# Kernel tuning notes

Measured on AMD Instinct MI355X. Metric: run time of the kernel, lower is better.

The kernel has to match this reference:

```python
import jax, jax.numpy as jnp
import numpy as np

INF_NUMBER = 1.0e12
ZERO_TOL = 1e-9
NEG_SLOPE = 0.2

B, G, N = 16, 128, 512
P, E, K, F = 4, 1, 3, 128


def setup_inputs() -> dict:
    key = jax.random.key(0)
    k1, k2, k3, k4, k5, k6, k7 = jax.random.split(key, 7)
    x = jax.random.normal(k1, (B, G, N), dtype=jnp.float32)
    u = jax.random.uniform(k2, (B, E, N, N), dtype=jnp.float32)
    S = jnp.where(u < 0.1, u, 0.0)
    std = 1.0 / np.sqrt(G * P)
    W = jax.random.uniform(k3, (P, E, G, G), minval=-std, maxval=std, dtype=jnp.float32)
    mixer = jax.random.uniform(k4, (P, E, 2 * F), minval=-std, maxval=std, dtype=jnp.float32)
    h = jax.random.uniform(k5, (P, F, E, K, G), minval=-std, maxval=std, dtype=jnp.float32)
    b = jax.random.uniform(k6, (F, 1), minval=-std, maxval=std, dtype=jnp.float32)
    return {"x": x, "S": S, "W": W, "mixer": mixer, "h": h, "b": b}


def _attention_gso(x, W, S):
    # x: (B,G,N); W: (P,E,G,G); S: (B,E,N,N)
    # Wx = W @ x_query : (B,P,E,G,N)
    Wx = jnp.einsum('pegh,bhn->bpegn', W, x)
    # xWx = x_key @ Wx : (B,P,E,N,N)  (x_key[b,m,g] = x[b,g,m])
    xWx = jnp.einsum('bgm,bpegn->bpemn', x, Wx)
    eij = jax.nn.leaky_relu(xWx, negative_slope=NEG_SLOPE)
    # edge mask from |S| summed over edge features: (B,1,1,N,N)
    mask = (jnp.sum(jnp.abs(S), axis=1) > ZERO_TOL).astype(x.dtype)[:, None, None]
    scores = eij * mask - (1.0 - mask) * INF_NUMBER
    aij = jax.nn.softmax(scores, axis=-1) * mask
    return aij  # (B,P,E,N,N)


def reference(x, S, W, mixer, h, b):
    # mixer is declared by the torch module but unused in key-query mode
    aij = _attention_gso(x, W, S)  # (B,P,E,N,N)
    # K-hop taps: z[k] = x @ aij^k, broadcast over (P,E)
    xk = jnp.broadcast_to(x[:, None, None], (B, P, E, G, N))
    taps = [xk]
    for _ in range(1, K):
        xk = jnp.einsum('bpegn,bpenm->bpegm', xk, aij)
        taps.append(xk)
    z = jnp.stack(taps, axis=3)  # (B,P,E,K,G,N)
    # filter GEMM: contract over (E,K,G) -> (B,P,F,N)
    y = jnp.einsum('bpekgn,pfekg->bpfn', z, h) + b  # b: (F,1) broadcasts
    # concatenate heads: relu then (B, P*F, N)
    y = jax.nn.relu(y)
    y = jnp.transpose(y, (0, 3, 1, 2)).reshape(B, N, P * F)
    return jnp.transpose(y, (0, 2, 1))
```

## Files before the change

kernel.cpp:

```cpp
#include <hip/hip_runtime.h>

#define Bx 16
#define Gx 128
#define Nx 512
#define Px 4
#define Kx 3
#define Fx 128
#define NEG_SLOPE 0.2f
#define ZERO_TOL 1e-9f
#define BIGF 1.0e30f

typedef unsigned short u16;
typedef unsigned int u32;
typedef __bf16 v8bf __attribute__((ext_vector_type(8)));
typedef _Float16 v8hf __attribute__((ext_vector_type(8)));
typedef float v4f __attribute__((ext_vector_type(4)));

__device__ __forceinline__ u16 f2b(float f) {
  union { float f; u32 u; } v; v.f = f;
  u32 r = (v.u + 0x7fffu + ((v.u >> 16) & 1u)) >> 16;
  return (u16)r;
}
__device__ __forceinline__ u16 f2h(float f) {
  union { _Float16 h; u16 u; } v; v.h = (_Float16)f;
  return v.u;
}

#define G2L16(gsrc, ldst)                                                     \
  __builtin_amdgcn_global_load_lds(                                           \
      (const __attribute__((address_space(1))) void*)(gsrc),                  \
      (__attribute__((address_space(3))) void*)(ldst), 16, 0, 0)

__global__ __launch_bounds__(256) void mask_kernel(const float* __restrict__ S,
                                                   u32* __restrict__ mb) {
  const int wi = blockIdx.x * 256 + threadIdx.x;
  const float4* S4 = (const float4*)S;
  u32 bits = 0;
#pragma unroll
  for (int q = 0; q < 8; q++) {
    float4 v = S4[(size_t)wi * 8 + q];
    bits |= (fabsf(v.x) > ZERO_TOL ? 1u : 0u) << (q * 4);
    bits |= (fabsf(v.y) > ZERO_TOL ? 2u : 0u) << (q * 4);
    bits |= (fabsf(v.z) > ZERO_TOL ? 4u : 0u) << (q * 4);
    bits |= (fabsf(v.w) > ZERO_TOL ? 8u : 0u) << (q * 4);
  }
  mb[wi] = bits;
}

__global__ __launch_bounds__(256) void castx3_kernel(const float* __restrict__ x,
                                                     u16* __restrict__ xb,
                                                     u16* __restrict__ xTb,
                                                     u16* __restrict__ xT16) {
  const int b = blockIdx.z, g0 = blockIdx.x * 32, n0 = blockIdx.y * 32;
  const int tid = threadIdx.x;
  __shared__ float t[32][33];
  const int r = tid >> 3, c4 = (tid & 7) * 4;
  const float* xp = x + (size_t)b * Gx * Nx;
  float4 v = *(const float4*)&xp[(g0 + r) * Nx + n0 + c4];
  ushort4 o;
  o.x = f2b(v.x); o.y = f2b(v.y); o.z = f2b(v.z); o.w = f2b(v.w);
  *(ushort4*)&xb[(size_t)b * Gx * Nx + (g0 + r) * Nx + n0 + c4] = o;
  t[r][c4 + 0] = v.x; t[r][c4 + 1] = v.y; t[r][c4 + 2] = v.z; t[r][c4 + 3] = v.w;
  __syncthreads();
  float tv[4] = {t[c4 + 0][r], t[c4 + 1][r], t[c4 + 2][r], t[c4 + 3][r]};
  ushort4 ob, oh;
  ob.x = f2b(tv[0]); oh.x = f2h(tv[0]);
  ob.y = f2b(tv[1]); oh.y = f2h(tv[1]);
  ob.z = f2b(tv[2]); oh.z = f2h(tv[2]);
  ob.w = f2b(tv[3]); oh.w = f2h(tv[3]);
  size_t off = (size_t)b * Nx * Gx + (size_t)(n0 + r) * Gx + g0 + c4;
  *(ushort4*)&xTb[off] = ob;
  *(ushort4*)&xT16[off] = oh;
}

__global__ __launch_bounds__(256) void castw16_kernel(const float* __restrict__ W,
                                                      u16* __restrict__ w16) {
  int i4 = (blockIdx.x * 256 + threadIdx.x) * 4;
  float4 v = *(const float4*)&W[i4];
  ushort4 o;
  o.x = f2h(v.x); o.y = f2h(v.y); o.z = f2h(v.z); o.w = f2h(v.w);
  *(ushort4*)&w16[i4] = o;
}

__global__ __launch_bounds__(256) void casth_kernel(const float* __restrict__ h,
                                                    u16* __restrict__ Hb) {
  int i4 = (blockIdx.x * 256 + threadIdx.x) * 4;
  float4 v = *(const float4*)&h[i4];
  ushort4 o;
  o.x = f2b(v.x); o.y = f2b(v.y); o.z = f2b(v.z); o.w = f2b(v.w);
  *(ushort4*)&Hb[i4] = o;
}

__global__ __launch_bounds__(256) void wxt16_kernel(const u16* __restrict__ xT16,
                                                    const u16* __restrict__ w16,
                                                    u16* __restrict__ WxT16) {
  __shared__ __align__(16) char smem[49152];
  constexpr int OB = 16384;
  const int bp = blockIdx.x, b = bp >> 2, p = bp & 3;
  const int rt = blockIdx.y;
  const int tid = threadIdx.x;
  const int w = tid >> 6, l = tid & 63;
  const int wr = w >> 1, wc = w & 1;
  const int lr = l & 15, ks = l >> 4;

  const u16* Ap = xT16 + ((size_t)b * Nx + rt * 64) * Gx;
  const u16* Bp = w16 + (size_t)p * Gx * Gx;
#pragma unroll
  for (int it = 0; it < 4; it++) {
    int chunk = it * 256 + w * 64 + l;
    int r = chunk >> 4, kq = l & 15;
    int kg = (kq ^ (r & 15)) * 8;
    G2L16(Ap + (size_t)r * Gx + kg, smem + it * 4096 + w * 1024);
  }
#pragma unroll
  for (int it = 0; it < 8; it++) {
    int chunk = it * 256 + w * 64 + l;
    int r = chunk >> 4, kq = l & 15;
    int kg = (kq ^ (r & 15)) * 8;
    G2L16(Bp + (size_t)r * Gx + kg, smem + OB + it * 4096 + w * 1024);
  }
  __syncthreads();

  v4f acc[2][4];
#pragma unroll
  for (int fr = 0; fr < 2; fr++)
#pragma unroll
    for (int fc = 0; fc < 4; fc++) acc[fr][fc] = (v4f){0.f, 0.f, 0.f, 0.f};

#pragma unroll
  for (int t = 0; t < 4; t++) {
    int kk = t * 4 + ks;
    v8hf ah[2];
#pragma unroll
    for (int fr = 0; fr < 2; fr++) {
      int ra = wr * 32 + fr * 16 + lr;
      ah[fr] = *(const v8hf*)(smem + ra * 256 + ((kk ^ (ra & 15)) * 16));
    }
#pragma unroll
    for (int fc = 0; fc < 4; fc++) {
      int rb = wc * 64 + fc * 16 + lr;
      v8hf bh = *(const v8hf*)(smem + OB + rb * 256 + ((kk ^ (rb & 15)) * 16));
#pragma unroll
      for (int fr = 0; fr < 2; fr++)
        acc[fr][fc] = __builtin_amdgcn_mfma_f32_16x16x32_f16(ah[fr], bh, acc[fr][fc], 0, 0, 0);
    }
  }

  u16* op = WxT16 + (size_t)bp * Nx * Gx;
#pragma unroll
  for (int fr = 0; fr < 2; fr++)
#pragma unroll
    for (int fc = 0; fc < 4; fc++) {
      int n = rt * 64 + wr * 32 + fr * 16 + ks * 4;
      int g = wc * 64 + fc * 16 + lr;
#pragma unroll
      for (int q = 0; q < 4; q++) op[(size_t)(n + q) * Gx + g] = f2h(acc[fr][fc][q]);
    }
}

__global__ __launch_bounds__(512) void attn4_kernel(const u16* __restrict__ xT16,
                                                    const u16* __restrict__ WxT16,
                                                    const u32* __restrict__ mb,
                                                    u16* __restrict__ aijT) {
  __shared__ __align__(16) char smem[55296];
  constexpr int OB = 16384, OMBS = 49152, ORED = 53248;
  const int bp = blockIdx.x, b = bp >> 2;
  const int i0 = blockIdx.y * 64;
  const int tid = threadIdx.x;
  const int w = tid >> 6, l = tid & 63;
  const int wr = w >> 2, wc = w & 3;
  const int lr = l & 15, ks = l >> 4;

  {
    const u32* mbp = mb + ((size_t)b * Nx + i0) * 16;
    u32* mbs = (u32*)(smem + OMBS);
    mbs[tid] = mbp[tid];
    mbs[tid + 512] = mbp[tid + 512];
  }
  {
    const u16* Ap = xT16 + ((size_t)b * Nx + i0) * Gx;
#pragma unroll
    for (int it = 0; it < 2; it++) {
      int chunk = it * 512 + w * 64 + l;
      int r = chunk >> 4, kq = l & 15;
      int kg = (kq ^ (r & 15)) * 8;
      G2L16(Ap + (size_t)r * Gx + kg, smem + it * 8192 + w * 1024);
    }
  }

  v4f acc[2][8];
#pragma unroll
  for (int fr = 0; fr < 2; fr++)
#pragma unroll
    for (int fc = 0; fc < 8; fc++) acc[fr][fc] = (v4f){0.f, 0.f, 0.f, 0.f};

  const u16* Bp = WxT16 + (size_t)bp * Nx * Gx;
  for (int g0 = 0; g0 < Gx; g0 += 32) {
    __syncthreads();
#pragma unroll
    for (int it = 0; it < 4; it++) {
      int chunk = it * 512 + w * 64 + l;
      int r = chunk >> 2, kq = l & 3;
      int kg = (kq ^ (r & 3)) * 8;
      G2L16(Bp + (size_t)r * Gx + g0 + kg, smem + OB + it * 8192 + w * 1024);
    }
    __syncthreads();
    int kk = (g0 >> 3) + ks;
    v8hf ah[2];
#pragma unroll
    for (int fr = 0; fr < 2; fr++) {
      int ra = wr * 32 + fr * 16 + lr;
      ah[fr] = *(const v8hf*)(smem + ra * 256 + ((kk ^ (ra & 15)) * 16));
    }
#pragma unroll
    for (int fc = 0; fc < 8; fc++) {
      int rb = wc * 128 + fc * 16 + lr;
      v8hf bh = *(const v8hf*)(smem + OB + rb * 64 + ((ks ^ (rb & 3)) * 16));
#pragma unroll
      for (int fr = 0; fr < 2; fr++)
        acc[fr][fc] = __builtin_amdgcn_mfma_f32_16x16x32_f16(ah[fr], bh, acc[fr][fc], 0, 0, 0);
    }
  }

  u32* mbs = (u32*)(smem + OMBS);
  float* red0 = (float*)(smem + ORED);
  float* red1 = red0 + 256;

#pragma unroll
  for (int fr = 0; fr < 2; fr++)
#pragma unroll
    for (int q = 0; q < 4; q++) {
      int row = wr * 32 + fr * 16 + ks * 4 + q;
      float m = -BIGF;
#pragma unroll
      for (int fc = 0; fc < 8; fc++) {
        u32 word = mbs[row * 16 + wc * 4 + (fc >> 1)];
        int bit = ((fc & 1) << 4) + lr;
        float v = acc[fr][fc][q];
        v = v >= 0.f ? v : NEG_SLOPE * v;
        v = ((word >> bit) & 1u) ? v : -BIGF;
        acc[fr][fc][q] = v;
        m = fmaxf(m, v);
      }
      m = fmaxf(m, __shfl_xor(m, 1, 64));
      m = fmaxf(m, __shfl_xor(m, 2, 64));
      m = fmaxf(m, __shfl_xor(m, 4, 64));
      m = fmaxf(m, __shfl_xor(m, 8, 64));
      if (lr == 0) red0[row * 4 + wc] = m;
    }
  __syncthreads();
#pragma unroll
  for (int fr = 0; fr < 2; fr++)
#pragma unroll
    for (int q = 0; q < 4; q++) {
      int row = wr * 32 + fr * 16 + ks * 4 + q;
      float4 pm = *(const float4*)&red0[row * 4];
      float gm = fmaxf(fmaxf(pm.x, pm.y), fmaxf(pm.z, pm.w));
      float s = 0.f;
#pragma unroll
      for (int fc = 0; fc < 8; fc++) {
        float v = acc[fr][fc][q];
        float e = (v <= -0.5f * BIGF) ? 0.f : __expf(v - gm);
        acc[fr][fc][q] = e;
        s += e;
      }
      s += __shfl_xor(s, 1, 64);
      s += __shfl_xor(s, 2, 64);
      s += __shfl_xor(s, 4, 64);
      s += __shfl_xor(s, 8, 64);
      if (lr == 0) red1[row * 4 + wc] = s;
    }
  __syncthreads();
  u16* dst = aijT + (size_t)bp * Nx * Nx + i0;
#pragma unroll
  for (int fr = 0; fr < 2; fr++) {
    int rbase = wr * 32 + fr * 16 + ks * 4;
    float inv[4];
#pragma unroll
    for (int q = 0; q < 4; q++) {
      float4 ps = *(const float4*)&red1[(rbase + q) * 4];
      float tot = (ps.x + ps.y) + (ps.z + ps.w);
      inv[q] = tot > 0.f ? 1.f / tot : 0.f;
    }
#pragma unroll
    for (int fc = 0; fc < 8; fc++) {
      int j = wc * 128 + fc * 16 + lr;
      ushort4 pk;
      pk.x = f2b(acc[fr][fc][0] * inv[0]);
      pk.y = f2b(acc[fr][fc][1] * inv[1]);
      pk.z = f2b(acc[fr][fc][2] * inv[2]);
      pk.w = f2b(acc[fr][fc][3] * inv[3]);
      *(ushort4*)&dst[(size_t)j * Nx + rbase] = pk;
    }
  }
}

template <int MODE>
__global__ __launch_bounds__(256) void gnt_kernel(const u16* __restrict__ pA,
                                                  const u16* __restrict__ pB,
                                                  const u16* __restrict__ pC,
                                                  const u16* __restrict__ pHb,
                                                  u16* __restrict__ o1,
                                                  u16* __restrict__ o2,
                                                  float* __restrict__ oF,
                                                  const float* __restrict__ bias) {
  __shared__ __align__(16) char smem[4096 + 8192];
  const int bp = blockIdx.x;
  const int b = bp >> 2, p = bp & 3;
  const int by = blockIdx.y;
  const int rt = (MODE == 1) ? (by >> 2) : by;
  const int ct = (MODE == 1) ? (by & 3) : 0;
  const int tid = threadIdx.x;
  const int w = tid >> 6, l = tid & 63;
  const int wr = w >> 1, wc = w & 1;
  const int lr = l & 15, kslot = l >> 4;

  constexpr int KTOT = (MODE == 2) ? (Kx * Gx) : Nx;
  constexpr int SA = (MODE == 2) ? Gx : Nx;
  constexpr int SB = (MODE == 2) ? (Kx * Gx) : Nx;

  const u16* Abase;
  const u16* Bbase;
  if (MODE == 0) {
    Abase = pA + (size_t)bp * Nx * Nx + (size_t)rt * 64 * Nx;
    Bbase = pB + (size_t)b * Gx * Nx;
  } else if (MODE == 1) {
    Abase = pA + (size_t)bp * Gx * Nx + (size_t)rt * 64 * Nx;
    Bbase = pB + (size_t)bp * Nx * Nx + (size_t)ct * 128 * Nx;
  } else {
    Abase = nullptr;
    Bbase = pHb + (size_t)p * Fx * (Kx * Gx);
  }

  const int sar = tid >> 2, sakq = tid & 3;
  const int sakg = sakq ^ (sar & 3);
  const int sbr0 = tid >> 2, sbkg0 = (tid & 3) ^ (sbr0 & 3);
  const int sbr1 = (tid + 256) >> 2, sbkg1 = (tid & 3) ^ (sbr1 & 3);
  char* ldsAdst = smem + w * 1024;
  char* ldsBdst0 = smem + 4096 + w * 1024;
  char* ldsBdst1 = smem + 4096 + 4096 + w * 1024;

  int aoff[2], boff[4];
#pragma unroll
  for (int fr = 0; fr < 2; fr++) {
    int row = wr * 32 + fr * 16 + lr;
    aoff[fr] = row * 64 + ((kslot ^ (row & 3)) * 16);
  }
#pragma unroll
  for (int fc = 0; fc < 4; fc++) {
    int row = wc * 64 + fc * 16 + lr;
    boff[fc] = 4096 + row * 64 + ((kslot ^ (row & 3)) * 16);
  }

  v4f acc[2][4];
#pragma unroll
  for (int fr = 0; fr < 2; fr++)
#pragma unroll
    for (int fc = 0; fc < 4; fc++) acc[fr][fc] = (v4f){0.f, 0.f, 0.f, 0.f};

  for (int k0 = 0; k0 < KTOT; k0 += 32) {
    const u16* Aseg;
    int kin;
    if (MODE == 2) {
      int seg = k0 >> 7;
      kin = k0 & 127;
      const u16* base = (seg == 0) ? (pA + (size_t)b * Nx * Gx)
                       : (seg == 1) ? (pB + (size_t)bp * Nx * Gx)
                                    : (pC + (size_t)bp * Nx * Gx);
      Aseg = base + (size_t)rt * 64 * Gx;
    } else {
      Aseg = Abase;
      kin = k0;
    }
    __syncthreads();
    G2L16(Aseg + (size_t)sar * SA + kin + sakg * 8, ldsAdst);
    G2L16(Bbase + (size_t)sbr0 * SB + k0 + sbkg0 * 8, ldsBdst0);
    G2L16(Bbase + (size_t)sbr1 * SB + k0 + sbkg1 * 8, ldsBdst1);
    __syncthreads();

    v8bf af[2], bf4[4];
#pragma unroll
    for (int fr = 0; fr < 2; fr++) af[fr] = *(const v8bf*)(smem + aoff[fr]);
#pragma unroll
    for (int fc = 0; fc < 4; fc++) bf4[fc] = *(const v8bf*)(smem + boff[fc]);
#pragma unroll
    for (int fr = 0; fr < 2; fr++)
#pragma unroll
      for (int fc = 0; fc < 4; fc++)
        acc[fr][fc] = __builtin_amdgcn_mfma_f32_16x16x32_bf16(af[fr], bf4[fc],
                                                              acc[fr][fc], 0, 0, 0);
  }

  if (MODE == 0) {
    u16* z1p = o1 + (size_t)bp * Gx * Nx;
    u16* z1Tp = o2 + (size_t)bp * Nx * Gx;
#pragma unroll
    for (int fr = 0; fr < 2; fr++)
#pragma unroll
      for (int fc = 0; fc < 4; fc++) {
        int m0 = rt * 64 + wr * 32 + fr * 16 + kslot * 4;
        int g = wc * 64 + fc * 16 + lr;
        v4f a = acc[fr][fc];
        ushort4 pk;
        pk.x = f2b(a[0]); pk.y = f2b(a[1]); pk.z = f2b(a[2]); pk.w = f2b(a[3]);
        *(ushort4*)&z1p[(size_t)g * Nx + m0] = pk;
        z1Tp[(size_t)(m0 + 0) * Gx + g] = pk.x;
        z1Tp[(size_t)(m0 + 1) * Gx + g] = pk.y;
        z1Tp[(size_t)(m0 + 2) * Gx + g] = pk.z;
        z1Tp[(size_t)(m0 + 3) * Gx + g] = pk.w;
      }
  } else if (MODE == 1) {
    u16* z2Tp = o1 + (size_t)bp * Nx * Gx;
#pragma unroll
    for (int fr = 0; fr < 2; fr++)
#pragma unroll
      for (int fc = 0; fc < 4; fc++) {
        int g0r = rt * 64 + wr * 32 + fr * 16 + kslot * 4;
        int m = ct * 128 + wc * 64 + fc * 16 + lr;
        v4f a = acc[fr][fc];
        ushort4 pk;
        pk.x = f2b(a[0]); pk.y = f2b(a[1]); pk.z = f2b(a[2]); pk.w = f2b(a[3]);
        *(ushort4*)&z2Tp[(size_t)m * Gx + g0r] = pk;
      }
  } else {
    float* op = oF + (size_t)(b * Px + p) * Fx * Nx;
#pragma unroll
    for (int fc = 0; fc < 4; fc++) {
      int f = wc * 64 + fc * 16 + lr;
      float bi = bias[f];
#pragma unroll
      for (int fr = 0; fr < 2; fr++) {
        int n0 = rt * 64 + wr * 32 + fr * 16 + kslot * 4;
        v4f a = acc[fr][fc];
        float4 o;
        o.x = fmaxf(a[0] + bi, 0.f);
        o.y = fmaxf(a[1] + bi, 0.f);
        o.z = fmaxf(a[2] + bi, 0.f);
        o.w = fmaxf(a[3] + bi, 0.f);
        *(float4*)&op[(size_t)f * Nx + n0] = o;
      }
    }
  }
}

extern "C" void kernel_launch(void* const* d_in, const int* in_sizes, int n_in,
                              void* d_out, int out_size, void* d_ws, size_t ws_size,
                              hipStream_t stream) {
  const float* x = (const float*)d_in[0];
  const float* S = (const float*)d_in[1];
  const float* W = (const float*)d_in[2];
  const float* h = (const float*)d_in[4];
  const float* bias = (const float*)d_in[5];
  float* out = (float*)d_out;

  char* ws = (char*)d_ws;
  u16* aijT  = (u16*)ws;
  u16* WxT16 = (u16*)(ws + 33554432);
  u16* xT16  = (u16*)(ws + 41943040);
  u16* xTb   = (u16*)(ws + 44040192);
  u16* xb    = (u16*)(ws + 46137344);
  u16* z1    = (u16*)(ws + 48234496);
  u16* z1T   = (u16*)(ws + 56623104);
  u16* z2T   = (u16*)(ws + 65011712);
  u16* Hb    = (u16*)(ws + 73400320);
  u16* W16   = (u16*)(ws + 73793536);
  u32* mb    = (u32*)(ws + 73924608);

  mask_kernel<<<dim3((Bx * Nx * Nx / 32) / 256), 256, 0, stream>>>(S, mb);
  castx3_kernel<<<dim3(Gx / 32, Nx / 32, Bx), 256, 0, stream>>>(x, xb, xTb, xT16);
  castw16_kernel<<<dim3(Px * Gx * Gx / 1024), 256, 0, stream>>>(W, W16);
  casth_kernel<<<dim3(Px * Fx * Kx * Gx / 1024), 256, 0, stream>>>(h, Hb);
  wxt16_kernel<<<dim3(Bx * Px, Nx / 64), 256, 0, stream>>>(xT16, W16, WxT16);
  attn4_kernel<<<dim3(Bx * Px, Nx / 64), 512, 0, stream>>>(xT16, WxT16, mb, aijT);
  gnt_kernel<0><<<dim3(Bx * Px, 8), 256, 0, stream>>>(aijT, xb, nullptr, nullptr,
                                                      z1, z1T, nullptr, nullptr);
  gnt_kernel<1><<<dim3(Bx * Px, 8), 256, 0, stream>>>(z1, aijT, nullptr, nullptr,
                                                      z2T, nullptr, nullptr, nullptr);
  gnt_kernel<2><<<dim3(Bx * Px, 8), 256, 0, stream>>>(xTb, z1T, z2T, Hb,
                                                      nullptr, nullptr, out, bias);
  (void)in_sizes; (void)n_in; (void)out_size; (void)ws_size;
}
```

Baseline: 81.24 us.

## Merge prep kernels into one launch and double-buffer LDS in GEMM kernels

Four small preprocessing kernels (mask bits, x casts and transposes, W and h casts) are merged into a single launch, with the role chosen by block index, to cut launch overhead and tail gaps between them. The gnt GEMM kernels move from a single LDS buffer to two ping-pong buffers, so the async global-to-LDS loads for the next K tile are issued before computing on the current one, leaving one barrier per iteration. This doubles LDS use per block, which may lower occupancy, and overlap depends on how the compiler places the waits for the async loads.

```diff
diff --git a/kernel.cpp b/kernel.cpp
--- a/kernel.cpp
+++ b/kernel.cpp
@@ -31,64 +31,65 @@
       (const __attribute__((address_space(1))) void*)(gsrc),                  \
       (__attribute__((address_space(3))) void*)(ldst), 16, 0, 0)
 
-__global__ __launch_bounds__(256) void mask_kernel(const float* __restrict__ S,
-                                                   u32* __restrict__ mb) {
-  const int wi = blockIdx.x * 256 + threadIdx.x;
-  const float4* S4 = (const float4*)S;
-  u32 bits = 0;
-#pragma unroll
-  for (int q = 0; q < 8; q++) {
-    float4 v = S4[(size_t)wi * 8 + q];
-    bits |= (fabsf(v.x) > ZERO_TOL ? 1u : 0u) << (q * 4);
-    bits |= (fabsf(v.y) > ZERO_TOL ? 2u : 0u) << (q * 4);
-    bits |= (fabsf(v.z) > ZERO_TOL ? 4u : 0u) << (q * 4);
-    bits |= (fabsf(v.w) > ZERO_TOL ? 8u : 0u) << (q * 4);
-  }
-  mb[wi] = bits;
-}
-
-__global__ __launch_bounds__(256) void castx3_kernel(const float* __restrict__ x,
-                                                     u16* __restrict__ xb,
-                                                     u16* __restrict__ xTb,
-                                                     u16* __restrict__ xT16) {
-  const int b = blockIdx.z, g0 = blockIdx.x * 32, n0 = blockIdx.y * 32;
+__global__ __launch_bounds__(256) void prep_kernel(const float* __restrict__ S,
+                                                   const float* __restrict__ x,
+                                                   const float* __restrict__ W,
+                                                   const float* __restrict__ h,
+                                                   u32* __restrict__ mb,
+                                                   u16* __restrict__ xb,
+                                                   u16* __restrict__ xTb,
+                                                   u16* __restrict__ xT16,
+                                                   u16* __restrict__ w16,
+                                                   u16* __restrict__ Hb) {
+  const int blk = blockIdx.x;
   const int tid = threadIdx.x;
   __shared__ float t[32][33];
-  const int r = tid >> 3, c4 = (tid & 7) * 4;
-  const float* xp = x + (size_t)b * Gx * Nx;
-  float4 v = *(const float4*)&xp[(g0 + r) * Nx + n0 + c4];
-  ushort4 o;
-  o.x = f2b(v.x); o.y = f2b(v.y); o.z = f2b(v.z); o.w = f2b(v.w);
-  *(ushort4*)&xb[(size_t)b * Gx * Nx + (g0 + r) * Nx + n0 + c4] = o;
-  t[r][c4 + 0] = v.x; t[r][c4 + 1] = v.y; t[r][c4 + 2] = v.z; t[r][c4 + 3] = v.w;
-  __syncthreads();
-  float tv[4] = {t[c4 + 0][r], t[c4 + 1][r], t[c4 + 2][r], t[c4 + 3][r]};
-  ushort4 ob, oh;
-  ob.x = f2b(tv[0]); oh.x = f2h(tv[0]);
-  ob.y = f2b(tv[1]); oh.y = f2h(tv[1]);
-  ob.z = f2b(tv[2]); oh.z = f2h(tv[2]);
-  ob.w = f2b(tv[3]); oh.w = f2h(tv[3]);
-  size_t off = (size_t)b * Nx * Gx + (size_t)(n0 + r) * Gx + g0 + c4;
-  *(ushort4*)&xTb[off] = ob;
-  *(ushort4*)&xT16[off] = oh;
-}
-
-__global__ __launch_bounds__(256) void castw16_kernel(const float* __restrict__ W,
-                                                      u16* __restrict__ w16) {
-  int i4 = (blockIdx.x * 256 + threadIdx.x) * 4;
-  float4 v = *(const float4*)&W[i4];
-  ushort4 o;
-  o.x = f2h(v.x); o.y = f2h(v.y); o.z = f2h(v.z); o.w = f2h(v.w);
-  *(ushort4*)&w16[i4] = o;
-}
-
-__global__ __launch_bounds__(256) void casth_kernel(const float* __restrict__ h,
-                                                    u16* __restrict__ Hb) {
-  int i4 = (blockIdx.x * 256 + threadIdx.x) * 4;
-  float4 v = *(const float4*)&h[i4];
-  ushort4 o;
-  o.x = f2b(v.x); o.y = f2b(v.y); o.z = f2b(v.z); o.w = f2b(v.w);
-  *(ushort4*)&Hb[i4] = o;
+  if (blk < 512) {
+    const int wi = blk * 256 + tid;
+    const float4* S4 = (const float4*)S;
+    u32 bits = 0;
+#pragma unroll
+    for (int q = 0; q < 8; q++) {
+      float4 v = S4[(size_t)wi * 8 + q];
+      bits |= (fabsf(v.x) > ZERO_TOL ? 1u : 0u) << (q * 4);
+      bits |= (fabsf(v.y) > ZERO_TOL ? 2u : 0u) << (q * 4);
+      bits |= (fabsf(v.z) > ZERO_TOL ? 4u : 0u) << (q * 4);
+      bits |= (fabsf(v.w) > ZERO_TOL ? 8u : 0u) << (q * 4);
+    }
+    mb[wi] = bits;
+  } else if (blk < 1536) {
+    const int idx = blk - 512;
+    const int b = idx >> 6, g0 = ((idx >> 4) & 3) * 32, n0 = (idx & 15) * 32;
+    const int r = tid >> 3, c4 = (tid & 7) * 4;
+    const float* xp = x + (size_t)b * Gx * Nx;
+    float4 v = *(const float4*)&xp[(g0 + r) * Nx + n0 + c4];
+    ushort4 o;
+    o.x = f2b(v.x); o.y = f2b(v.y); o.z = f2b(v.z); o.w = f2b(v.w);
+    *(ushort4*)&xb[(size_t)b * Gx * Nx + (g0 + r) * Nx + n0 + c4] = o;
+    t[r][c4 + 0] = v.x; t[r][c4 + 1] = v.y; t[r][c4 + 2] = v.z; t[r][c4 + 3] = v.w;
+    __syncthreads();
+    float tv[4] = {t[c4 + 0][r], t[c4 + 1][r], t[c4 + 2][r], t[c4 + 3][r]};
+    ushort4 ob, oh;
+    ob.x = f2b(tv[0]); oh.x = f2h(tv[0]);
+    ob.y = f2b(tv[1]); oh.y = f2h(tv[1]);
+    ob.z = f2b(tv[2]); oh.z = f2h(tv[2]);
+    ob.w = f2b(tv[3]); oh.w = f2h(tv[3]);
+    size_t off = (size_t)b * Nx * Gx + (size_t)(n0 + r) * Gx + g0 + c4;
+    *(ushort4*)&xTb[off] = ob;
+    *(ushort4*)&xT16[off] = oh;
+  } else if (blk < 1600) {
+    int i4 = ((blk - 1536) * 256 + tid) * 4;
+    float4 v = *(const float4*)&W[i4];
+    ushort4 o;
+    o.x = f2h(v.x); o.y = f2h(v.y); o.z = f2h(v.z); o.w = f2h(v.w);
+    *(ushort4*)&w16[i4] = o;
+  } else {
+    int i4 = ((blk - 1600) * 256 + tid) * 4;
+    float4 v = *(const float4*)&h[i4];
+    ushort4 o;
+    o.x = f2b(v.x); o.y = f2b(v.y); o.z = f2b(v.z); o.w = f2b(v.w);
+    *(ushort4*)&Hb[i4] = o;
+  }
 }
 
 __global__ __launch_bounds__(256) void wxt16_kernel(const u16* __restrict__ xT16,
@@ -304,7 +305,7 @@
                                                   u16* __restrict__ o2,
                                                   float* __restrict__ oF,
                                                   const float* __restrict__ bias) {
-  __shared__ __align__(16) char smem[4096 + 8192];
+  __shared__ __align__(16) char smem[2][12288];
   const int bp = blockIdx.x;
   const int b = bp >> 2, p = bp & 3;
   const int by = blockIdx.y;
@@ -318,6 +319,7 @@
   constexpr int KTOT = (MODE == 2) ? (Kx * Gx) : Nx;
   constexpr int SA = (MODE == 2) ? Gx : Nx;
   constexpr int SB = (MODE == 2) ? (Kx * Gx) : Nx;
+  constexpr int NT = KTOT / 32;
 
   const u16* Abase;
   const u16* Bbase;
@@ -332,13 +334,10 @@
     Bbase = pHb + (size_t)p * Fx * (Kx * Gx);
   }
 
-  const int sar = tid >> 2, sakq = tid & 3;
-  const int sakg = sakq ^ (sar & 3);
+  const int sar = tid >> 2;
+  const int sakg = (tid & 3) ^ (sar & 3);
   const int sbr0 = tid >> 2, sbkg0 = (tid & 3) ^ (sbr0 & 3);
   const int sbr1 = (tid + 256) >> 2, sbkg1 = (tid & 3) ^ (sbr1 & 3);
-  char* ldsAdst = smem + w * 1024;
-  char* ldsBdst0 = smem + 4096 + w * 1024;
-  char* ldsBdst1 = smem + 4096 + 4096 + w * 1024;
 
   int aoff[2], boff[4];
 #pragma unroll
@@ -352,13 +351,7 @@
     boff[fc] = 4096 + row * 64 + ((kslot ^ (row & 3)) * 16);
   }
 
-  v4f acc[2][4];
-#pragma unroll
-  for (int fr = 0; fr < 2; fr++)
-#pragma unroll
-    for (int fc = 0; fc < 4; fc++) acc[fr][fc] = (v4f){0.f, 0.f, 0.f, 0.f};
-
-  for (int k0 = 0; k0 < KTOT; k0 += 32) {
+  auto STAGE = [&](int bufi, int k0) {
     const u16* Aseg;
     int kin;
     if (MODE == 2) {
@@ -372,23 +365,36 @@
       Aseg = Abase;
       kin = k0;
     }
+    char* base = smem[bufi];
+    G2L16(Aseg + (size_t)sar * SA + kin + sakg * 8, base + w * 1024);
+    G2L16(Bbase + (size_t)sbr0 * SB + k0 + sbkg0 * 8, base + 4096 + w * 1024);
+    G2L16(Bbase + (size_t)sbr1 * SB + k0 + sbkg1 * 8, base + 8192 + w * 1024);
+  };
+
+  v4f acc[2][4];
+#pragma unroll
+  for (int fr = 0; fr < 2; fr++)
+#pragma unroll
+    for (int fc = 0; fc < 4; fc++) acc[fr][fc] = (v4f){0.f, 0.f, 0.f, 0.f};
+
+  STAGE(0, 0);
+  int cur = 0;
+  for (int t = 0; t < NT; t++) {
     __syncthreads();
-    G2L16(Aseg + (size_t)sar * SA + kin + sakg * 8, ldsAdst);
-    G2L16(Bbase + (size_t)sbr0 * SB + k0 + sbkg0 * 8, ldsBdst0);
-    G2L16(Bbase + (size_t)sbr1 * SB + k0 + sbkg1 * 8, ldsBdst1);
-    __syncthreads();
-
+    if (t + 1 < NT) STAGE(cur ^ 1, (t + 1) * 32);
+    const char* bb = smem[cur];
     v8bf af[2], bf4[4];
 #pragma unroll
-    for (int fr = 0; fr < 2; fr++) af[fr] = *(const v8bf*)(smem + aoff[fr]);
-#pragma unroll
-    for (int fc = 0; fc < 4; fc++) bf4[fc] = *(const v8bf*)(smem + boff[fc]);
+    for (int fr = 0; fr < 2; fr++) af[fr] = *(const v8bf*)(bb + aoff[fr]);
+#pragma unroll
+    for (int fc = 0; fc < 4; fc++) bf4[fc] = *(const v8bf*)(bb + boff[fc]);
 #pragma unroll
     for (int fr = 0; fr < 2; fr++)
 #pragma unroll
       for (int fc = 0; fc < 4; fc++)
         acc[fr][fc] = __builtin_amdgcn_mfma_f32_16x16x32_bf16(af[fr], bf4[fc],
                                                               acc[fr][fc], 0, 0, 0);
+    cur ^= 1;
   }
 
   if (MODE == 0) {
@@ -466,10 +472,7 @@
   u16* W16   = (u16*)(ws + 73793536);
   u32* mb    = (u32*)(ws + 73924608);
 
-  mask_kernel<<<dim3((Bx * Nx * Nx / 32) / 256), 256, 0, stream>>>(S, mb);
-  castx3_kernel<<<dim3(Gx / 32, Nx / 32, Bx), 256, 0, stream>>>(x, xb, xTb, xT16);
-  castw16_kernel<<<dim3(Px * Gx * Gx / 1024), 256, 0, stream>>>(W, W16);
-  casth_kernel<<<dim3(Px * Fx * Kx * Gx / 1024), 256, 0, stream>>>(h, Hb);
+  prep_kernel<<<dim3(1792), 256, 0, stream>>>(S, x, W, h, mb, xb, xTb, xT16, W16, Hb);
   wxt16_kernel<<<dim3(Bx * Px, Nx / 64), 256, 0, stream>>>(xT16, W16, WxT16);
   attn4_kernel<<<dim3(Bx * Px, Nx / 64), 512, 0, stream>>>(xT16, WxT16, mb, aijT);
   gnt_kernel<0><<<dim3(Bx * Px, 8), 256, 0, stream>>>(aijT, xb, nullptr, nullptr,
```

After: 77.14 us. 5.1% less time.
